# Kernel tuning notes

Hardware: AMD Instinct MI355X
Metric: run time of the kernel (lower is better)

The kernel has to match this reference:

```python
import jax, jax.numpy as jnp
import numpy as np

MAX_LEN = 2048
D_MODEL = 1024
NUM_HEADS = 16
D_HEAD = D_MODEL // NUM_HEADS
BATCH = 2
SEQ = 2048


def setup_inputs() -> dict:
    key = jax.random.key(0)
    ks = jax.random.split(key, 8)
    scale = 1.0 / np.sqrt(D_MODEL)
    return {
        "x": jax.random.normal(ks[0], (BATCH, SEQ, D_MODEL), dtype=jnp.float32),
        "Wq": jax.random.normal(ks[1], (D_MODEL, D_MODEL), dtype=jnp.float32) * scale,
        "bq": jnp.zeros((D_MODEL,), dtype=jnp.float32),
        "Wk": jax.random.normal(ks[2], (D_MODEL, D_MODEL), dtype=jnp.float32) * scale,
        "bk": jnp.zeros((D_MODEL,), dtype=jnp.float32),
        "Wv": jax.random.normal(ks[3], (D_MODEL, D_MODEL), dtype=jnp.float32) * scale,
        "bv": jnp.zeros((D_MODEL,), dtype=jnp.float32),
        "Er": jax.random.normal(ks[4], (MAX_LEN, D_HEAD), dtype=jnp.float32),
    }


def _skew(QEr):
    # QEr: [B, H, S, S] -> Transformer-XL skew -> Srel: [B, H, S, S]
    B, H, S, _ = QEr.shape
    padded = jnp.pad(QEr, ((0, 0), (0, 0), (0, 0), (1, 0)))  # [B,H,S,S+1]
    reshaped = padded.reshape(B, H, S + 1, S)
    return reshaped[:, :, 1:, :]


def reference(x, Wq, bq, Wk, bk, Wv, bv, Er):
    B, S, D = x.shape
    H, dh = NUM_HEADS, D // NUM_HEADS
    q = (x @ Wq + bq).reshape(B, S, H, dh).transpose(0, 2, 1, 3)  # [B,H,S,dh]
    k = (x @ Wk + bk).reshape(B, S, H, dh).transpose(0, 2, 1, 3)
    v = (x @ Wv + bv).reshape(B, S, H, dh).transpose(0, 2, 1, 3)
    Er_s = Er[MAX_LEN - S:, :]                                    # [S, dh]
    QEr = jnp.einsum("bhsd,ld->bhsl", q, Er_s)                    # [B,H,S,S]
    Srel = _skew(QEr)
    QKt = jnp.einsum("bhsd,bhtd->bhst", q, k)
    attn = (QKt + Srel) / jnp.sqrt(jnp.asarray(dh, x.dtype))
    causal = jnp.tril(jnp.ones((S, S), dtype=bool))
    attn = jnp.where(causal[None, None], attn, -jnp.inf)
    attn = jax.nn.softmax(attn, axis=-1)
    out = jnp.einsum("bhst,bhtd->bhsd", attn, v)                  # [B,H,S,dh]
    return out.transpose(0, 2, 1, 3).reshape(B, S, D)             # dropout in eval = identity
```

## Files before the change

kernel.cpp:

```cpp
#include <hip/hip_runtime.h>
#include <hip/hip_bf16.h>

#define SLEN   2048
#define DMODEL 1024
#define NHEADS 16
#define DHEAD  64
#define NBATCH 2
#define EPAD_ROWS 2432

#define QSCALE 0.18033688011112042f
#define EXPB   23.083120654223414f

typedef __bf16 bf16x8 __attribute__((ext_vector_type(8)));
typedef float  f32x4  __attribute__((ext_vector_type(4)));

__device__ __forceinline__ unsigned short f2bf(float f) {
    unsigned int u = __builtin_bit_cast(unsigned int, f);
    return (unsigned short)((u + 0x7fffu + ((u >> 16) & 1u)) >> 16);
}

__device__ __forceinline__ unsigned short f2bf_hw(float f) {
    return __builtin_bit_cast(unsigned short, (__bf16)f);
}

__device__ __forceinline__ float exp2_hw(float x) {
    float r;
    asm("v_exp_f32 %0, %1" : "=v"(r) : "v"(x));
    return r;
}

__device__ __forceinline__ bf16x8 ld8(const unsigned short* p) {
    union { uint4 u; bf16x8 b; } t;
    t.u = *(const uint4*)p;
    return t.b;
}

__device__ __forceinline__ void glds16(const unsigned short* g, unsigned short* l) {
    __builtin_amdgcn_global_load_lds(
        (const __attribute__((address_space(1))) unsigned int*)g,
        (__attribute__((address_space(3))) unsigned int*)l, 16, 0, 0);
}

__global__ __launch_bounds__(256) void prep_kernel(
    const float* __restrict__ x, const float* __restrict__ Er,
    const float* __restrict__ Wq, const float* __restrict__ Wk,
    const float* __restrict__ Wv,
    unsigned short* __restrict__ xb, unsigned short* __restrict__ Ep,
    unsigned short* __restrict__ Wt) {
    const int bi = blockIdx.x, tid = threadIdx.x;
    if (bi < 4096) {
        int i = (bi * 256 + tid) * 4;
        float4 v = *(const float4*)(x + i);
        ushort4 o;
        o.x = f2bf(v.x); o.y = f2bf(v.y); o.z = f2bf(v.z); o.w = f2bf(v.w);
        *(ushort4*)(xb + i) = o;
    } else if (bi < 4704) {
        int i = (bi - 4096) * 256 + tid;
        int row = i >> 6;
        unsigned short v = 0;
        if (row < SLEN) v = f2bf(Er[i]);
        Ep[i] = v;
    } else {
        __shared__ float tile[32][33];
        const int b3 = bi - 4704;
        const int z = b3 >> 10, rem = b3 & 1023;
        const int n0 = (rem & 31) * 32, k0 = (rem >> 5) * 32;
        const float* W = (z == 0) ? Wq : (z == 1 ? Wk : Wv);
        unsigned short* out = Wt + (size_t)z * DMODEL * DMODEL;
        const int tx = tid & 31, ty = tid >> 5;
        for (int r = 0; r < 32; r += 8)
            tile[ty + r][tx] = W[(size_t)(k0 + ty + r) * DMODEL + n0 + tx];
        __syncthreads();
        for (int r = 0; r < 32; r += 8)
            out[(size_t)(n0 + ty + r) * DMODEL + k0 + tx] = f2bf(tile[tx][ty + r]);
    }
}

__global__ __launch_bounds__(256, 3) void qkv_gemm(
    const unsigned short* __restrict__ xb, const unsigned short* __restrict__ Wt,
    const float* __restrict__ bq, const float* __restrict__ bk, const float* __restrict__ bv,
    unsigned short* __restrict__ Qs, unsigned short* __restrict__ Ks,
    unsigned short* __restrict__ Vts) {
    const int b = blockIdx.x;
    const int x7 = b & 7, s = b >> 3;
    const int mt = ((x7 >> 1) << 3) | (s & 7);
    const int ntile = ((x7 & 1) << 2) | ((s >> 3) & 3);
    const int z = s >> 5;
    const int m0 = mt * 128, n0 = ntile * 128;

    const float* bias = (z == 0) ? bq : (z == 1 ? bk : bv);
    const unsigned short* Wz = Wt + (size_t)z * DMODEL * DMODEL;

    __shared__ __align__(16) unsigned short As[128][64];
    __shared__ __align__(16) unsigned short Bs[128][64];

    const int tid = threadIdx.x;
    const int wave = tid >> 6, lane = tid & 63, l16 = lane & 15, quad = lane >> 4;
    const int wm = (wave >> 1) * 64, wn = (wave & 1) * 64;

    const int lr8 = lane >> 3;
    const int sc  = ((lane & 7) ^ lr8) * 8;

    f32x4 acc[4][4];
#pragma unroll
    for (int mi = 0; mi < 4; mi++)
#pragma unroll
        for (int ni = 0; ni < 4; ni++) acc[mi][ni] = (f32x4){0.f, 0.f, 0.f, 0.f};

    for (int j = 0; j < 16; ++j) {
        if (j) __syncthreads();
        const int k0 = j * 64;
#pragma unroll
        for (int c = 0; c < 4; c++) {
            const int seg = wave * 4 + c;
            const int r8  = seg * 8 + lr8;
            glds16(&xb[(size_t)(m0 + r8) * DMODEL + k0 + sc], &As[seg * 8][0]);
            glds16(&Wz[(size_t)(n0 + r8) * DMODEL + k0 + sc], &Bs[seg * 8][0]);
        }
        __syncthreads();

        const unsigned short (*Aarr)[64] = (z == 2) ? Bs : As;
        const unsigned short (*Barr)[64] = (z == 2) ? As : Bs;
#pragma unroll
        for (int ks = 0; ks < 2; ks++) {
            const int pc = ((ks * 4 + quad) ^ (l16 & 7)) * 8;
            bf16x8 a[4], bb[4];
#pragma unroll
            for (int mi = 0; mi < 4; mi++) a[mi] = ld8(&Aarr[wm + mi * 16 + l16][pc]);
#pragma unroll
            for (int ni = 0; ni < 4; ni++) bb[ni] = ld8(&Barr[wn + ni * 16 + l16][pc]);
#pragma unroll
            for (int mi = 0; mi < 4; mi++)
#pragma unroll
                for (int ni = 0; ni < 4; ni++)
                    acc[mi][ni] = __builtin_amdgcn_mfma_f32_16x16x32_bf16(a[mi], bb[ni], acc[mi][ni], 0, 0, 0);
        }
    }

    if (z == 2) {
#pragma unroll
        for (int mi = 0; mi < 4; mi++)
#pragma unroll
            for (int r = 0; r < 4; r++) {
                const int n = n0 + wm + mi * 16 + quad * 4 + r;
                const float bb = bias[n];
                const int h = n >> 6, d = n & 63;
#pragma unroll
                for (int ni = 0; ni < 4; ni++) {
                    const int m = m0 + wn + ni * 16 + l16;
                    const int bi = m >> 11, ss = m & 2047;
                    Vts[((size_t)((bi * NHEADS + h) * 64 + d)) * SLEN + ss] = f2bf(acc[mi][ni][r] + bb);
                }
            }
    } else {
#pragma unroll
        for (int ni = 0; ni < 4; ni++) {
            const int n = n0 + wn + ni * 16 + l16;
            const float bb = bias[n];
            const int h = n >> 6, d = n & 63;
#pragma unroll
            for (int mi = 0; mi < 4; mi++)
#pragma unroll
                for (int r = 0; r < 4; r++) {
                    const int m = m0 + wm + mi * 16 + quad * 4 + r;
                    const int bi = m >> 11, ss = m & 2047;
                    float v = acc[mi][ni][r] + bb;
                    if (z == 0)
                        Qs[((size_t)(bi * NHEADS + h) * SLEN + ss) * 64 + d] = f2bf(v * QSCALE);
                    else
                        Ks[((size_t)(bi * NHEADS + h) * SLEN + ss) * 64 + d] = f2bf(v);
                }
        }
    }
}

__global__ __launch_bounds__(256, 2) void attn_kernel(
    const unsigned short* __restrict__ Q,
    const unsigned short* __restrict__ K,
    const unsigned short* __restrict__ Vt,
    const unsigned short* __restrict__ Ep,
    float* __restrict__ out) {
    const int tid = threadIdx.x;
    const int wave = tid >> 6, lane = tid & 63, l16 = lane & 15, quad = lane >> 4;
    const int lr8 = lane >> 3;
    const int swz = ((lane & 7) ^ lr8) * 8;

    const int bh = blockIdx.x & 31;
    const int pg = blockIdx.x >> 5;

    __shared__ __align__(16) unsigned short Ksh[2][64 * 64];
    __shared__ __align__(16) unsigned short Vsh[2][64 * 64];
    __shared__ __align__(16) unsigned short Esh[256 * 64];
    __shared__ __align__(16) unsigned short Pg[4][16][88];

    const unsigned short* Qb = Q + (size_t)bh * SLEN * 64;
    const unsigned short* Kb = K + (size_t)bh * SLEN * 64;
    const unsigned short* Vb = Vt + (size_t)bh * 64 * SLEN;
    const int ob = bh >> 4, oh = bh & 15;

    const int pc0 = (quad ^ (l16 & 7)) * 8;
    const int pc1 = ((4 + quad) ^ (l16 & 7)) * 8;
    int perm[4];
    bool hi[4];
#pragma unroll
    for (int r = 0; r < 4; r++) {
        const int row16 = quad * 4 + r;
        perm[r] = (quad << 4) | ((l16 + 15 - row16) & 15);
        hi[r] = (l16 + row16 >= 15);
    }

    int s0 = pg * 64;
    int ntp = pg + 1;

#pragma unroll 1
    for (int pass = 0; pass < 2; ++pass) {
        const int sw = s0 + 16 * wave;
        const bf16x8 aq0 = ld8(Qb + (size_t)(sw + l16) * 64 + quad * 8);
        const bf16x8 aq1 = ld8(Qb + (size_t)(sw + l16) * 64 + 32 + quad * 8);

        f32x4 accO[4];
        float sacc[4];
#pragma unroll
        for (int nt = 0; nt < 4; nt++) accO[nt] = (f32x4){0.f, 0.f, 0.f, 0.f};
#pragma unroll
        for (int r = 0; r < 4; r++) sacc[r] = 0.f;

        const int p0row = SLEN - 64 - s0;

#pragma unroll
        for (int c = 0; c < 2; c++) {
            const int seg = wave * 2 + c;
            glds16(&Kb[(size_t)(seg * 8 + lr8) * 64 + swz], &Ksh[0][seg * 8 * 64]);
            glds16(&Vb[(size_t)(seg * 8 + lr8) * SLEN + swz], &Vsh[0][seg * 8 * 64]);
        }
#pragma unroll
        for (int u = 0; u < 6; u++) {
            const int idx = wave * 6 + u;
            const int grow = p0row + idx * 8;
            glds16(&Ep[(size_t)(grow + lr8) * 64 + swz], &Esh[(grow & 255) * 64]);
        }
        __syncthreads();

        for (int j = 0; j < ntp; ++j) {
            const int t0 = j * 64;
            const int cur = j & 1;

            if (j + 1 < ntp) {
                const int t1 = t0 + 64, nb = cur ^ 1;
#pragma unroll
                for (int c = 0; c < 2; c++) {
                    const int seg = wave * 2 + c;
                    glds16(&Kb[(size_t)(t1 + seg * 8 + lr8) * 64 + swz], &Ksh[nb][seg * 8 * 64]);
                    glds16(&Vb[(size_t)(seg * 8 + lr8) * SLEN + t1 + swz], &Vsh[nb][seg * 8 * 64]);
                }
                const int er = p0row + t0 + 128;
#pragma unroll
                for (int c = 0; c < 2; c++) {
                    const int seg = wave * 2 + c;
                    glds16(&Ep[(size_t)(er + seg * 8 + lr8) * 64 + swz],
                           &Esh[((er + seg * 8) & 255) * 64]);
                }
            }

            f32x4 accS[4];
#pragma unroll
            for (int nt = 0; nt < 4; nt++)
                accS[nt] = (f32x4){-EXPB, -EXPB, -EXPB, -EXPB};
#pragma unroll
            for (int nt = 0; nt < 4; nt++) {
                bf16x8 bk0 = ld8(&Ksh[cur][(nt * 16 + l16) * 64 + pc0]);
                bf16x8 bk1 = ld8(&Ksh[cur][(nt * 16 + l16) * 64 + pc1]);
                accS[nt] = __builtin_amdgcn_mfma_f32_16x16x32_bf16(aq0, bk0, accS[nt], 0, 0, 0);
                accS[nt] = __builtin_amdgcn_mfma_f32_16x16x32_bf16(aq1, bk1, accS[nt], 0, 0, 0);
            }

            const int rm0 = (SLEN - 16 - sw + t0) & 255;
            f32x4 accE[5];
#pragma unroll
            for (int nt = 0; nt < 5; nt++) accE[nt] = (f32x4){0.f, 0.f, 0.f, 0.f};
#pragma unroll
            for (int nt = 0; nt < 5; nt++) {
                const int rowm = (rm0 + nt * 16 + l16) & 255;
                bf16x8 be0 = ld8(&Esh[rowm * 64 + pc0]);
                bf16x8 be1 = ld8(&Esh[rowm * 64 + pc1]);
                accE[nt] = __builtin_amdgcn_mfma_f32_16x16x32_bf16(aq0, be0, accE[nt], 0, 0, 0);
                accE[nt] = __builtin_amdgcn_mfma_f32_16x16x32_bf16(aq1, be1, accE[nt], 0, 0, 0);
            }

            auto scoreblk = [&](bool masked) {
#pragma unroll
                for (int nt = 0; nt < 4; nt++) {
#pragma unroll
                    for (int r = 0; r < 4; r++) {
                        float send = hi[r] ? accE[nt][r] : accE[nt + 1][r];
                        float rel = __shfl(send, perm[r]);
                        float pexp = exp2_hw(accS[nt][r] + rel);
                        if (masked)
                            pexp = (t0 + nt * 16 + l16 <= sw + quad * 4 + r) ? pexp : 0.0f;
                        sacc[r] += pexp;
                        Pg[wave][quad * 4 + r][nt * 16 + l16] = f2bf_hw(pexp);
                    }
                }
            };
            if (t0 + 63 <= sw) scoreblk(false);
            else               scoreblk(true);

            bf16x8 a0 = ld8(&Pg[wave][l16][quad * 8]);
            bf16x8 a1 = ld8(&Pg[wave][l16][32 + quad * 8]);
#pragma unroll
            for (int nt = 0; nt < 4; nt++) {
                bf16x8 bv0 = ld8(&Vsh[cur][(nt * 16 + l16) * 64 + pc0]);
                bf16x8 bv1 = ld8(&Vsh[cur][(nt * 16 + l16) * 64 + pc1]);
                accO[nt] = __builtin_amdgcn_mfma_f32_16x16x32_bf16(a0, bv0, accO[nt], 0, 0, 0);
                accO[nt] = __builtin_amdgcn_mfma_f32_16x16x32_bf16(a1, bv1, accO[nt], 0, 0, 0);
            }

            __syncthreads();
        }

#pragma unroll
        for (int r = 0; r < 4; r++) {
            float s4 = sacc[r];
#pragma unroll
            for (int off = 1; off < 16; off <<= 1) s4 += __shfl_xor(s4, off);
            const float inv = 1.f / s4;
            const int s = sw + quad * 4 + r;
#pragma unroll
            for (int nt = 0; nt < 4; nt++)
                out[((size_t)(ob * SLEN + s)) * DMODEL + oh * 64 + nt * 16 + l16] =
                    accO[nt][r] * inv;
        }

        s0 = (31 - pg) * 64;
        ntp = 32 - pg;
    }
}

extern "C" void kernel_launch(void* const* d_in, const int* in_sizes, int n_in,
                              void* d_out, int out_size, void* d_ws, size_t ws_size,
                              hipStream_t stream) {
    const float* x  = (const float*)d_in[0];
    const float* Wq = (const float*)d_in[1];
    const float* bq = (const float*)d_in[2];
    const float* Wk = (const float*)d_in[3];
    const float* bk = (const float*)d_in[4];
    const float* Wv = (const float*)d_in[5];
    const float* bv = (const float*)d_in[6];
    const float* Er = (const float*)d_in[7];
    float* out = (float*)d_out;

    char* p = (char*)d_ws;
    unsigned short* xb  = (unsigned short*)p; p += (size_t)4096 * 1024 * 2;
    unsigned short* Wt  = (unsigned short*)p; p += (size_t)3 * 1024 * 1024 * 2;
    unsigned short* Qs  = (unsigned short*)p; p += (size_t)32 * 2048 * 64 * 2;
    unsigned short* Ks  = (unsigned short*)p; p += (size_t)32 * 2048 * 64 * 2;
    unsigned short* Vts = (unsigned short*)p; p += (size_t)32 * 2048 * 64 * 2;
    unsigned short* Ep  = (unsigned short*)p; p += (size_t)EPAD_ROWS * 64 * 2;

    hipLaunchKernelGGL(prep_kernel, dim3(7776), dim3(256), 0, stream,
                       x, Er, Wq, Wk, Wv, xb, Ep, Wt);
    hipLaunchKernelGGL(qkv_gemm, dim3(768), dim3(256), 0, stream,
                       xb, Wt, bq, bk, bv, Qs, Ks, Vts);
    hipLaunchKernelGGL(attn_kernel, dim3(512), dim3(256), 0, stream, Qs, Ks, Vts, Ep, out);
}
```

Measured before the change: 177.4 us.

## Transpose MFMA operands to keep P in registers, dropping the LDS round-trip

Swaps the A/B operands of the QK^T, QEr and PV MFMAs so the score tile comes out transposed, with each lane holding one query row's values. P is then packed to bf16 with v_cvt_pk_bf16_f32 and rearranged with permlane16/32 swaps into the PV operand layout. This removes the per-wave Pg shared-memory write/read and makes the row-sum reduction and the output stores (float4) simpler. In exchange it adds a register rotation of the Er accumulators, new shuffle index maths for the relative-position skew, and more cross-lane permute instructions, with correctness risk in the new indexing.

```diff
diff --git a/kernel.cpp b/kernel.cpp
--- a/kernel.cpp
+++ b/kernel.cpp
@@ -19,14 +19,16 @@
     return (unsigned short)((u + 0x7fffu + ((u >> 16) & 1u)) >> 16);
 }
 
-__device__ __forceinline__ unsigned short f2bf_hw(float f) {
-    return __builtin_bit_cast(unsigned short, (__bf16)f);
-}
-
 __device__ __forceinline__ float exp2_hw(float x) {
     float r;
     asm("v_exp_f32 %0, %1" : "=v"(r) : "v"(x));
     return r;
+}
+
+__device__ __forceinline__ unsigned int cvtpk_bf16(float lo, float hi) {
+    unsigned int d;
+    asm("v_cvt_pk_bf16_f32 %0, %1, %2" : "=v"(d) : "v"(lo), "v"(hi));
+    return d;
 }
 
 __device__ __forceinline__ bf16x8 ld8(const unsigned short* p) {
@@ -191,7 +193,6 @@
     __shared__ __align__(16) unsigned short Ksh[2][64 * 64];
     __shared__ __align__(16) unsigned short Vsh[2][64 * 64];
     __shared__ __align__(16) unsigned short Esh[256 * 64];
-    __shared__ __align__(16) unsigned short Pg[4][16][88];
 
     const unsigned short* Qb = Q + (size_t)bh * SLEN * 64;
     const unsigned short* Kb = K + (size_t)bh * SLEN * 64;
@@ -200,13 +201,16 @@
 
     const int pc0 = (quad ^ (l16 & 7)) * 8;
     const int pc1 = ((4 + quad) ^ (l16 & 7)) * 8;
-    int perm[4];
-    bool hi[4];
+    const int krot = (15 - l16) & 3;
+    const bool c1 = (krot & 1) != 0, c2 = (krot & 2) != 0;
+    int permE[4]; bool hiE[4];
 #pragma unroll
     for (int r = 0; r < 4; r++) {
-        const int row16 = quad * 4 + r;
-        perm[r] = (quad << 4) | ((l16 + 15 - row16) & 15);
-        hi[r] = (l16 + row16 >= 15);
+        const int idx = quad * 4 + r + 15 - l16;
+        permE[r] = ((idx >> 2) & 3) * 16 + l16;
+        const int c  = r + 15 - l16;
+        const int qv = (quad - (c >> 2)) & 3;
+        hiE[r] = (qv * 4 + c) >= 16;
     }
 
     int s0 = pg * 64;
@@ -270,8 +274,8 @@
             for (int nt = 0; nt < 4; nt++) {
                 bf16x8 bk0 = ld8(&Ksh[cur][(nt * 16 + l16) * 64 + pc0]);
                 bf16x8 bk1 = ld8(&Ksh[cur][(nt * 16 + l16) * 64 + pc1]);
-                accS[nt] = __builtin_amdgcn_mfma_f32_16x16x32_bf16(aq0, bk0, accS[nt], 0, 0, 0);
-                accS[nt] = __builtin_amdgcn_mfma_f32_16x16x32_bf16(aq1, bk1, accS[nt], 0, 0, 0);
+                accS[nt] = __builtin_amdgcn_mfma_f32_16x16x32_bf16(bk0, aq0, accS[nt], 0, 0, 0);
+                accS[nt] = __builtin_amdgcn_mfma_f32_16x16x32_bf16(bk1, aq1, accS[nt], 0, 0, 0);
             }
 
             const int rm0 = (SLEN - 16 - sw + t0) & 255;
@@ -283,52 +287,82 @@
                 const int rowm = (rm0 + nt * 16 + l16) & 255;
                 bf16x8 be0 = ld8(&Esh[rowm * 64 + pc0]);
                 bf16x8 be1 = ld8(&Esh[rowm * 64 + pc1]);
-                accE[nt] = __builtin_amdgcn_mfma_f32_16x16x32_bf16(aq0, be0, accE[nt], 0, 0, 0);
-                accE[nt] = __builtin_amdgcn_mfma_f32_16x16x32_bf16(aq1, be1, accE[nt], 0, 0, 0);
-            }
-
+                accE[nt] = __builtin_amdgcn_mfma_f32_16x16x32_bf16(be0, aq0, accE[nt], 0, 0, 0);
+                accE[nt] = __builtin_amdgcn_mfma_f32_16x16x32_bf16(be1, aq1, accE[nt], 0, 0, 0);
+            }
+
+            f32x4 rotE[5];
+#pragma unroll
+            for (int g = 0; g < 5; g++) {
+                f32x4 A = accE[g], t, rt;
+#pragma unroll
+                for (int r = 0; r < 4; r++) t[r] = c1 ? A[(r + 1) & 3] : A[r];
+#pragma unroll
+                for (int r = 0; r < 4; r++) rt[r] = c2 ? t[(r + 2) & 3] : t[r];
+                rotE[g] = rt;
+            }
+
+            float pe[4][4];
             auto scoreblk = [&](bool masked) {
 #pragma unroll
                 for (int nt = 0; nt < 4; nt++) {
 #pragma unroll
                     for (int r = 0; r < 4; r++) {
-                        float send = hi[r] ? accE[nt][r] : accE[nt + 1][r];
-                        float rel = __shfl(send, perm[r]);
-                        float pexp = exp2_hw(accS[nt][r] + rel);
+                        float send = hiE[r] ? rotE[nt + 1][r] : rotE[nt][r];
+                        float rel = __shfl(send, permE[r]);
+                        float p = exp2_hw(accS[nt][r] + rel);
                         if (masked)
-                            pexp = (t0 + nt * 16 + l16 <= sw + quad * 4 + r) ? pexp : 0.0f;
-                        sacc[r] += pexp;
-                        Pg[wave][quad * 4 + r][nt * 16 + l16] = f2bf_hw(pexp);
+                            p = (t0 + nt * 16 + quad * 4 + r <= sw + l16) ? p : 0.0f;
+                        sacc[r] += p;
+                        pe[nt][r] = p;
                     }
                 }
             };
             if (t0 + 63 <= sw) scoreblk(false);
             else               scoreblk(true);
 
-            bf16x8 a0 = ld8(&Pg[wave][l16][quad * 8]);
-            bf16x8 a1 = ld8(&Pg[wave][l16][32 + quad * 8]);
+            unsigned int w[4][2];
 #pragma unroll
             for (int nt = 0; nt < 4; nt++) {
-                bf16x8 bv0 = ld8(&Vsh[cur][(nt * 16 + l16) * 64 + pc0]);
-                bf16x8 bv1 = ld8(&Vsh[cur][(nt * 16 + l16) * 64 + pc1]);
-                accO[nt] = __builtin_amdgcn_mfma_f32_16x16x32_bf16(a0, bv0, accO[nt], 0, 0, 0);
-                accO[nt] = __builtin_amdgcn_mfma_f32_16x16x32_bf16(a1, bv1, accO[nt], 0, 0, 0);
+                w[nt][0] = cvtpk_bf16(pe[nt][0], pe[nt][1]);
+                w[nt][1] = cvtpk_bf16(pe[nt][2], pe[nt][3]);
+            }
+            bf16x8 pf[2];
+#pragma unroll
+            for (int c = 0; c < 2; c++) {
+                unsigned int a0 = w[2 * c][0], b0 = w[2 * c + 1][0];
+                unsigned int a1 = w[2 * c][1], b1 = w[2 * c + 1][1];
+                asm volatile("v_permlane32_swap_b32 %0, %1" : "+v"(a0), "+v"(b0));
+                asm volatile("v_permlane16_swap_b32 %0, %1" : "+v"(a0), "+v"(b0));
+                asm volatile("v_permlane32_swap_b32 %0, %1" : "+v"(a1), "+v"(b1));
+                asm volatile("v_permlane16_swap_b32 %0, %1" : "+v"(a1), "+v"(b1));
+                union { uint4 u; bf16x8 b; } t;
+                t.u = (uint4){a0, a1, b0, b1};
+                pf[c] = t.b;
+            }
+
+#pragma unroll
+            for (int ntd = 0; ntd < 4; ntd++) {
+                bf16x8 bv0 = ld8(&Vsh[cur][(ntd * 16 + l16) * 64 + pc0]);
+                bf16x8 bv1 = ld8(&Vsh[cur][(ntd * 16 + l16) * 64 + pc1]);
+                accO[ntd] = __builtin_amdgcn_mfma_f32_16x16x32_bf16(bv0, pf[0], accO[ntd], 0, 0, 0);
+                accO[ntd] = __builtin_amdgcn_mfma_f32_16x16x32_bf16(bv1, pf[1], accO[ntd], 0, 0, 0);
             }
 
             __syncthreads();
         }
 
-#pragma unroll
-        for (int r = 0; r < 4; r++) {
-            float s4 = sacc[r];
-#pragma unroll
-            for (int off = 1; off < 16; off <<= 1) s4 += __shfl_xor(s4, off);
-            const float inv = 1.f / s4;
-            const int s = sw + quad * 4 + r;
-#pragma unroll
-            for (int nt = 0; nt < 4; nt++)
-                out[((size_t)(ob * SLEN + s)) * DMODEL + oh * 64 + nt * 16 + l16] =
-                    accO[nt][r] * inv;
+        float s4 = (sacc[0] + sacc[1]) + (sacc[2] + sacc[3]);
+        s4 += __shfl_xor(s4, 16);
+        s4 += __shfl_xor(s4, 32);
+        const float inv = 1.f / s4;
+        const int srow = sw + l16;
+        float* orow = out + ((size_t)(ob * SLEN + srow)) * DMODEL + oh * 64 + quad * 4;
+#pragma unroll
+        for (int ntd = 0; ntd < 4; ntd++) {
+            float4 st = {accO[ntd][0] * inv, accO[ntd][1] * inv,
+                         accO[ntd][2] * inv, accO[ntd][3] * inv};
+            *(float4*)(orow + ntd * 16) = st;
         }
 
         s0 = (31 - pg) * 64;
```

After: 176.3 us. About the same (-0.6%).
